# Kernel tuning notes

Measured on AMD Instinct MI355X. Metric: run time of the kernel, lower is better.

Reference implementation:

```python
import jax, jax.numpy as jnp
import numpy as np

HIDDEN = 768
INTER = 2048
N_EXPERTS = 8
TOP_K = 2
SWIGLU_LIMIT = 7.0
N_TOK = 8192


def setup_inputs() -> dict:
    key = jax.random.key(0)
    k_x, k_r, k_gu, k_d = jax.random.split(key, 4)
    x = jax.random.normal(k_x, (N_TOK, HIDDEN), dtype=jnp.float32)
    router_w = jax.random.normal(k_r, (N_EXPERTS, HIDDEN), dtype=jnp.float32) * 0.02
    gate_up_proj = jax.random.normal(k_gu, (N_EXPERTS, 2 * INTER, HIDDEN), dtype=jnp.float32) * 0.02
    down_proj = jax.random.normal(k_d, (N_EXPERTS, HIDDEN, INTER), dtype=jnp.float32) * 0.02
    return {"x": x, "router_w": router_w, "gate_up_proj": gate_up_proj, "down_proj": down_proj}


def reference(x, router_w, gate_up_proj, down_proj):
    # router: [n_tok, E]
    router_logits = x @ router_w.T
    topk_vals, topk_idx = jax.lax.top_k(router_logits, TOP_K)  # [n_tok, k]
    topk_weights = jax.nn.softmax(topk_vals.astype(jnp.float32), axis=-1).astype(x.dtype)

    out = jnp.zeros_like(x)
    # Loop over the small fixed expert set; each expert is a dense GEMM over all
    # tokens, masked by its per-token routing weight (0 for unrouted tokens) —
    # identical math to the original gather/GEMM/scatter dispatch.
    for e in range(N_EXPERTS):
        # per-token weight for expert e (sums slots; each expert appears at most once per token)
        w_e = jnp.sum(jnp.where(topk_idx == e, topk_weights, 0.0), axis=-1)  # [n_tok]
        gate_up = x @ gate_up_proj[e].T  # [n_tok, 2*I]
        gate, up = jnp.split(gate_up, 2, axis=-1)
        up = jnp.minimum(up, SWIGLU_LIMIT)
        mlp_out = (jax.nn.silu(gate) * up) @ down_proj[e].T  # [n_tok, H]
        out = out + mlp_out * w_e[:, None]
    return out
```

## Files before the change

kernel.cpp:

```cpp
#include <hip/hip_runtime.h>
#include <hip/hip_bf16.h>

typedef unsigned short u16;
typedef unsigned int u32;
typedef short bf16x8 __attribute__((ext_vector_type(8)));
typedef float f32x4 __attribute__((ext_vector_type(4)));

#define NTOK 8192
#define HID 768
#define INTER 2048
#define NEXP 8

#define MFMA16(a, b, c) __builtin_amdgcn_mfma_f32_16x16x32_bf16(a, b, c, 0, 0, 0)
#define S_BARRIER() __builtin_amdgcn_s_barrier()
#define WAITVM(n) asm volatile("s_waitcnt vmcnt(" #n ")" ::: "memory")

__device__ __forceinline__ u16 f2bf(float f) {
    u32 u = __builtin_bit_cast(u32, f);
    u32 r = (u + 0x7FFFu + ((u >> 16) & 1u)) >> 16;
    return (u16)r;
}

__device__ __forceinline__ void gld16(const void* g, void* l) {
    __builtin_amdgcn_global_load_lds((const __attribute__((address_space(1))) void*)g,
                                     (__attribute__((address_space(3))) void*)l, 16, 0, 0);
}

__global__ __launch_bounds__(256) void zero_kernel(float4* out4, int n4) {
    int i = blockIdx.x * blockDim.x + threadIdx.x;
    float4 z = {0.f, 0.f, 0.f, 0.f};
    int stride = gridDim.x * blockDim.x;
    for (int k = i; k < n4; k += stride) out4[k] = z;
}

__global__ __launch_bounds__(256) void cvt_kernel(const float* __restrict__ src, u16* __restrict__ dst, int n8) {
    int i = blockIdx.x * blockDim.x + threadIdx.x;
    int stride = gridDim.x * blockDim.x;
    for (; i < n8; i += stride) {
        const float4* s = (const float4*)(src + (size_t)i * 8);
        float4 a = s[0], b = s[1];
        u16 r[8] = {f2bf(a.x), f2bf(a.y), f2bf(a.z), f2bf(a.w),
                    f2bf(b.x), f2bf(b.y), f2bf(b.z), f2bf(b.w)};
        *(uint4*)(dst + (size_t)i * 8) = *(const uint4*)r;
    }
}

__global__ __launch_bounds__(256) void router2(const float* __restrict__ x, const float* __restrict__ rw,
                                               u32* __restrict__ route, float* __restrict__ wslot) {
    int wv = threadIdx.x >> 6, ln = threadIdx.x & 63;
    int t = blockIdx.x * 4 + wv;
    if (t >= NTOK) return;
    float xr[12];
#pragma unroll
    for (int j = 0; j < 12; j++) xr[j] = x[(size_t)t * HID + ln + j * 64];
    float lg[NEXP];
#pragma unroll
    for (int e = 0; e < NEXP; e++) {
        float a = 0.f;
#pragma unroll
        for (int j = 0; j < 12; j++) a += xr[j] * rw[e * HID + ln + j * 64];
#pragma unroll
        for (int off = 32; off; off >>= 1) a += __shfl_xor(a, off);
        lg[e] = a;
    }
    int i0 = 0;
    float v0 = lg[0];
#pragma unroll
    for (int e = 1; e < NEXP; e++)
        if (lg[e] > v0) { v0 = lg[e]; i0 = e; }
    int i1 = -1;
    float v1 = -1e30f;
#pragma unroll
    for (int e = 0; e < NEXP; e++) {
        if (e == i0) continue;
        if (lg[e] > v1) { v1 = lg[e]; i1 = e; }
    }
    float w0 = 1.f / (1.f + __expf(v1 - v0));
    float w1 = 1.f - w0;
    if (ln == 0) {
        wslot[0 * NTOK + t] = w0;
        wslot[1 * NTOK + t] = w1;
        route[t] = (u32)i0 | ((u32)i1 << 8);
    }
}

__global__ __launch_bounds__(1024) void scatter_kernel(const u32* __restrict__ route, int* __restrict__ counts,
                                                       int* __restrict__ tokslot, int* __restrict__ ntiles,
                                                       int* __restrict__ tiledesc) {
    __shared__ int sc[NEXP][1024];
    int tid = threadIdx.x;
    u32 rt[8];
    int cnt[NEXP] = {0, 0, 0, 0, 0, 0, 0, 0};
#pragma unroll
    for (int k = 0; k < 8; k++) {
        rt[k] = route[tid * 8 + k];
        cnt[rt[k] & 255]++;
        cnt[(rt[k] >> 8) & 255]++;
    }
#pragma unroll
    for (int e = 0; e < NEXP; e++) sc[e][tid] = cnt[e];
    __syncthreads();
    for (int off = 1; off < 1024; off <<= 1) {
        int v[NEXP];
#pragma unroll
        for (int e = 0; e < NEXP; e++) v[e] = (tid >= off) ? sc[e][tid - off] : 0;
        __syncthreads();
#pragma unroll
        for (int e = 0; e < NEXP; e++)
            if (tid >= off) sc[e][tid] += v[e];
        __syncthreads();
    }
    int base[NEXP];
#pragma unroll
    for (int e = 0; e < NEXP; e++) base[e] = sc[e][tid] - cnt[e];
#pragma unroll
    for (int k = 0; k < 8; k++) {
        int t = tid * 8 + k;
        int e0 = rt[k] & 255, e1 = (rt[k] >> 8) & 255;
        tokslot[e0 * NTOK + base[e0]] = t;
        base[e0]++;
        tokslot[e1 * NTOK + base[e1]] = t | (1 << 16);
        base[e1]++;
    }
    if (tid == 0) {
        int tot = 0;
        for (int e = 0; e < NEXP; e++) {
            int c = sc[e][1023];
            counts[e] = c;
            int nt = (c + 255) >> 8;
            for (int q = 0; q < nt; q++) tiledesc[tot++] = (e << 8) | q;
        }
        ntiles[0] = tot;
    }
}


#define STG(d, kt)                                           \
    do {                                                     \
        char* base_ = lds + (d)*24576 + (tid << 4);          \
        size_t ko_ = (size_t)(kt)*64;                        \
        gld16(aP[0] + ko_, base_);                           \
        gld16(aP[1] + ko_, base_ + 4096);                    \
        gld16(aP[2] + ko_, base_ + 8192);                    \
        gld16(aP[3] + ko_, base_ + 12288);                   \
        gld16(bP[0] + ko_, base_ + 16384);                   \
        gld16(bP[1] + ko_, base_ + 20480);                   \
    } while (0)

#define PIPE_MB(NKT)                                                      \
    f32x4 acc[8][4];                                                      \
    _Pragma("unroll") for (int m_ = 0; m_ < 8; m_++)                      \
        _Pragma("unroll") for (int n_ = 0; n_ < 4; n_++) acc[m_][n_] = (f32x4)0.f; \
    const int sOff = ((g4 ^ (rsel & 3) ^ ((rsel >> 2) & 3)) << 4);        \
    const int aBase = (wr * 128 + rsel) * 64 + sOff;                      \
    const int bBase = 16384 + (wc * 64 + rsel) * 64 + sOff;               \
    STG(0, 0);                                                            \
    WAITVM(0);                                                            \
    S_BARRIER();                                                          \
    for (int t = 0; t < (NKT); ++t) {                                     \
        if (t + 1 < (NKT)) STG((t + 1) & 1, t + 1);                       \
        const char* Tb = lds + (t & 1) * 24576;                           \
        bf16x8 af[8], bfr[4];                                             \
        _Pragma("unroll") for (int m_ = 0; m_ < 8; m_++)                  \
            af[m_] = *(const bf16x8*)(Tb + aBase + m_ * 1024);            \
        _Pragma("unroll") for (int n_ = 0; n_ < 4; n_++)                  \
            bfr[n_] = *(const bf16x8*)(Tb + bBase + n_ * 1024);           \
        _Pragma("unroll") for (int m_ = 0; m_ < 8; m_++)                  \
            _Pragma("unroll") for (int n_ = 0; n_ < 4; n_++)              \
                acc[m_][n_] = MFMA16(af[m_], bfr[n_], acc[m_][n_]);       \
        WAITVM(0);                                                        \
        S_BARRIER();                                                      \
    }

__global__ __launch_bounds__(256, 2) void gateup_mb(const u16* __restrict__ xb, const u16* __restrict__ gub,
                                                    const int* __restrict__ counts,
                                                    const int* __restrict__ ntiles, const int* __restrict__ tiledesc,
                                                    const int* __restrict__ tokslot, u16* __restrict__ h) {
    if ((int)blockIdx.y >= ntiles[0]) return;
    int td = tiledesc[blockIdx.y];
    int e = td >> 8;
    int cnt = counts[e];
    int row0 = (td & 255) * 256;
    int c0 = blockIdx.x * 64;

    extern __shared__ char lds[];
    int tid = threadIdx.x;
    int wv = tid >> 6, ln = tid & 63;
    int wr = wv >> 1, wc = wv & 1;
    int rsel = ln & 15, g4 = ln >> 4;

    int srow = tid >> 2, sl = tid & 3;
    int sswz = ((sl ^ (srow & 3) ^ ((srow >> 2) & 3)) << 4);
    const char* aP[4];
    const char* bP[2];
#pragma unroll
    for (int c = 0; c < 4; c++) {
        int gr = row0 + c * 64 + srow;
        gr = gr < cnt ? gr : cnt - 1;
        int tok = tokslot[e * NTOK + gr] & 0xFFFF;
        aP[c] = (const char*)xb + (size_t)tok * (HID * 2) + sswz;
    }
#pragma unroll
    for (int c = 0; c < 2; c++) {
        int r = c * 64 + srow;
        int wi = r & 63;
        int b = (wi >> 5) * 2048 + c0 + (r >> 6) * 32 + (wi & 31);
        bP[c] = (const char*)gub + ((size_t)e * 4096 + b) * (HID * 2) + sswz;
    }

    PIPE_MB(HID / 32)

#pragma unroll
    for (int mg = 0; mg < 8; mg++) {
#pragma unroll
        for (int j = 0; j < 4; j++) {
            int gr = row0 + wr * 128 + mg * 16 + g4 * 4 + j;
            if (gr >= cnt) continue;
            int ts = tokslot[e * NTOK + gr];
            int tok = ts & 0xFFFF, slot = ts >> 16;
            u16* hrow = h + (size_t)(slot * NTOK + tok) * INTER;
#pragma unroll
            for (int n = 0; n < 2; n++) {
                float gv = acc[mg][n][j];
                float uv = fminf(acc[mg][n + 2][j], 7.0f);
                float sg = gv / (1.0f + __expf(-gv));
                hrow[c0 + wc * 32 + n * 16 + rsel] = f2bf(sg * uv);
            }
        }
    }
}

__global__ __launch_bounds__(256, 2) void down_mb(const u16* __restrict__ hb, const u16* __restrict__ dnb,
                                                  const int* __restrict__ counts,
                                                  const int* __restrict__ ntiles, const int* __restrict__ tiledesc,
                                                  const int* __restrict__ tokslot,
                                                  const float* __restrict__ wslot, float* __restrict__ out) {
    if ((int)blockIdx.y >= ntiles[0]) return;
    int td = tiledesc[blockIdx.y];
    int e = td >> 8;
    int cnt = counts[e];
    int row0 = (td & 255) * 256;
    int col0 = blockIdx.x * 128;

    extern __shared__ char lds[];
    int tid = threadIdx.x;
    int wv = tid >> 6, ln = tid & 63;
    int wr = wv >> 1, wc = wv & 1;
    int rsel = ln & 15, g4 = ln >> 4;

    int srow = tid >> 2, sl = tid & 3;
    int sswz = ((sl ^ (srow & 3) ^ ((srow >> 2) & 3)) << 4);
    const char* aP[4];
    const char* bP[2];
#pragma unroll
    for (int c = 0; c < 4; c++) {
        int gr = row0 + c * 64 + srow;
        gr = gr < cnt ? gr : cnt - 1;
        int ts = tokslot[e * NTOK + gr];
        aP[c] = (const char*)hb + (size_t)((ts >> 16) * NTOK + (ts & 0xFFFF)) * (INTER * 2) + sswz;
    }
#pragma unroll
    for (int c = 0; c < 2; c++) {
        int r = c * 64 + srow;
        bP[c] = (const char*)dnb + ((size_t)e * HID + col0 + r) * (INTER * 2) + sswz;
    }

    PIPE_MB(INTER / 32)

#pragma unroll
    for (int mg = 0; mg < 8; mg++) {
#pragma unroll
        for (int j = 0; j < 4; j++) {
            int gr = row0 + wr * 128 + mg * 16 + g4 * 4 + j;
            if (gr >= cnt) continue;
            int ts = tokslot[e * NTOK + gr];
            int tok = ts & 0xFFFF, slot = ts >> 16;
            float w = wslot[slot * NTOK + tok];
#pragma unroll
            for (int n = 0; n < 4; n++) {
                int col = col0 + wc * 64 + n * 16 + rsel;
                atomicAdd(&out[(size_t)tok * HID + col], w * acc[mg][n][j]);
            }
        }
    }
}

extern "C" void kernel_launch(void* const* d_in, const int* in_sizes, int n_in,
                              void* d_out, int out_size, void* d_ws, size_t ws_size,
                              hipStream_t stream) {
    const float* x = (const float*)d_in[0];
    const float* rw = (const float*)d_in[1];
    const float* gu = (const float*)d_in[2];
    const float* dn = (const float*)d_in[3];
    float* out = (float*)d_out;
    char* ws = (char*)d_ws;

    int* counts = (int*)(ws + 0);
    int* ntiles = (int*)(ws + 64);
    int* tiledesc = (int*)(ws + 128);
    int* tokslot = (int*)(ws + 512);
    float* wslot = (float*)(ws + 262656);
    u16* xb = (u16*)(ws + 328192);
    u16* gub = (u16*)(ws + 12911104);
    u16* dnb = (u16*)(ws + 63242752);
    u16* hb = (u16*)(ws + 88408576);
    u32* route = (u32*)(ws + 88408576);

    zero_kernel<<<1024, 256, 0, stream>>>((float4*)out, NTOK * HID / 4);
    cvt_kernel<<<2048, 256, 0, stream>>>(x, xb, NTOK * HID / 8);
    cvt_kernel<<<2048, 256, 0, stream>>>(gu, gub, NEXP * 2 * INTER * HID / 8);
    cvt_kernel<<<2048, 256, 0, stream>>>(dn, dnb, NEXP * HID * INTER / 8);
    router2<<<NTOK / 4, 256, 0, stream>>>(x, rw, route, wslot);
    scatter_kernel<<<1, 1024, 0, stream>>>(route, counts, tokslot, ntiles, tiledesc);
    gateup_mb<<<dim3(32, 72), 256, 49152, stream>>>(xb, gub, counts, ntiles, tiledesc, tokslot, hb);
    down_mb<<<dim3(6, 72), 256, 49152, stream>>>(hb, dnb, counts, ntiles, tiledesc, tokslot, wslot, out);
}
```

Before: 343.8 us.

## Fuse output zeroing into router, store h compactly per expert, raise occupancy

The separate output-zeroing kernel is removed, and each router wave now zeroes its token's output row. The intermediate h is stored in expert-sorted compact order, indexed by a per-expert base offset computed in the scatter kernel. Gate-up stores and down-proj A loads therefore become contiguous rows instead of tokslot-indirected scattered rows, and gate-up no longer reads tokslot in its epilogue. Launch bounds are raised to 3 blocks per CU, which may force register spilling given the 32 accumulator vectors per thread.

```diff
diff --git a/kernel.cpp b/kernel.cpp
--- a/kernel.cpp
+++ b/kernel.cpp
@@ -24,13 +24,6 @@
 __device__ __forceinline__ void gld16(const void* g, void* l) {
     __builtin_amdgcn_global_load_lds((const __attribute__((address_space(1))) void*)g,
                                      (__attribute__((address_space(3))) void*)l, 16, 0, 0);
-}
-
-__global__ __launch_bounds__(256) void zero_kernel(float4* out4, int n4) {
-    int i = blockIdx.x * blockDim.x + threadIdx.x;
-    float4 z = {0.f, 0.f, 0.f, 0.f};
-    int stride = gridDim.x * blockDim.x;
-    for (int k = i; k < n4; k += stride) out4[k] = z;
 }
 
 __global__ __launch_bounds__(256) void cvt_kernel(const float* __restrict__ src, u16* __restrict__ dst, int n8) {
@@ -45,11 +38,15 @@
     }
 }
 
-__global__ __launch_bounds__(256) void router2(const float* __restrict__ x, const float* __restrict__ rw,
-                                               u32* __restrict__ route, float* __restrict__ wslot) {
+__global__ __launch_bounds__(256) void router2z(const float* __restrict__ x, const float* __restrict__ rw,
+                                                u32* __restrict__ route, float* __restrict__ wslot,
+                                                float4* __restrict__ out4) {
     int wv = threadIdx.x >> 6, ln = threadIdx.x & 63;
     int t = blockIdx.x * 4 + wv;
     if (t >= NTOK) return;
+    float4 z = {0.f, 0.f, 0.f, 0.f};
+#pragma unroll
+    for (int k = 0; k < 3; k++) out4[(size_t)t * 192 + ln + k * 64] = z;
     float xr[12];
 #pragma unroll
     for (int j = 0; j < 12; j++) xr[j] = x[(size_t)t * HID + ln + j * 64];
@@ -86,7 +83,7 @@
 
 __global__ __launch_bounds__(1024) void scatter_kernel(const u32* __restrict__ route, int* __restrict__ counts,
                                                        int* __restrict__ tokslot, int* __restrict__ ntiles,
-                                                       int* __restrict__ tiledesc) {
+                                                       int* __restrict__ tiledesc, int* __restrict__ ebase) {
     __shared__ int sc[NEXP][1024];
     int tid = threadIdx.x;
     u32 rt[8];
@@ -123,10 +120,12 @@
         base[e1]++;
     }
     if (tid == 0) {
-        int tot = 0;
+        int tot = 0, b = 0;
         for (int e = 0; e < NEXP; e++) {
             int c = sc[e][1023];
             counts[e] = c;
+            ebase[e] = b;
+            b += c;
             int nt = (c + 255) >> 8;
             for (int q = 0; q < nt; q++) tiledesc[tot++] = (e << 8) | q;
         }
@@ -172,14 +171,16 @@
         S_BARRIER();                                                      \
     }
 
-__global__ __launch_bounds__(256, 2) void gateup_mb(const u16* __restrict__ xb, const u16* __restrict__ gub,
+__global__ __launch_bounds__(256, 3) void gateup_mb(const u16* __restrict__ xb, const u16* __restrict__ gub,
                                                     const int* __restrict__ counts,
                                                     const int* __restrict__ ntiles, const int* __restrict__ tiledesc,
-                                                    const int* __restrict__ tokslot, u16* __restrict__ h) {
+                                                    const int* __restrict__ tokslot, const int* __restrict__ ebase,
+                                                    u16* __restrict__ h) {
     if ((int)blockIdx.y >= ntiles[0]) return;
     int td = tiledesc[blockIdx.y];
     int e = td >> 8;
     int cnt = counts[e];
+    int eb = ebase[e];
     int row0 = (td & 255) * 256;
     int c0 = blockIdx.x * 64;
 
@@ -216,9 +217,7 @@
         for (int j = 0; j < 4; j++) {
             int gr = row0 + wr * 128 + mg * 16 + g4 * 4 + j;
             if (gr >= cnt) continue;
-            int ts = tokslot[e * NTOK + gr];
-            int tok = ts & 0xFFFF, slot = ts >> 16;
-            u16* hrow = h + (size_t)(slot * NTOK + tok) * INTER;
+            u16* hrow = h + (size_t)(eb + gr) * INTER;
 #pragma unroll
             for (int n = 0; n < 2; n++) {
                 float gv = acc[mg][n][j];
@@ -230,15 +229,16 @@
     }
 }
 
-__global__ __launch_bounds__(256, 2) void down_mb(const u16* __restrict__ hb, const u16* __restrict__ dnb,
+__global__ __launch_bounds__(256, 3) void down_mb(const u16* __restrict__ hb, const u16* __restrict__ dnb,
                                                   const int* __restrict__ counts,
                                                   const int* __restrict__ ntiles, const int* __restrict__ tiledesc,
-                                                  const int* __restrict__ tokslot,
+                                                  const int* __restrict__ tokslot, const int* __restrict__ ebase,
                                                   const float* __restrict__ wslot, float* __restrict__ out) {
     if ((int)blockIdx.y >= ntiles[0]) return;
     int td = tiledesc[blockIdx.y];
     int e = td >> 8;
     int cnt = counts[e];
+    int eb = ebase[e];
     int row0 = (td & 255) * 256;
     int col0 = blockIdx.x * 128;
 
@@ -256,8 +256,7 @@
     for (int c = 0; c < 4; c++) {
         int gr = row0 + c * 64 + srow;
         gr = gr < cnt ? gr : cnt - 1;
-        int ts = tokslot[e * NTOK + gr];
-        aP[c] = (const char*)hb + (size_t)((ts >> 16) * NTOK + (ts & 0xFFFF)) * (INTER * 2) + sswz;
+        aP[c] = (const char*)hb + (size_t)(eb + gr) * (INTER * 2) + sswz;
     }
 #pragma unroll
     for (int c = 0; c < 2; c++) {
@@ -298,6 +297,7 @@
     int* counts = (int*)(ws + 0);
     int* ntiles = (int*)(ws + 64);
     int* tiledesc = (int*)(ws + 128);
+    int* ebase = (int*)(ws + 448);
     int* tokslot = (int*)(ws + 512);
     float* wslot = (float*)(ws + 262656);
     u16* xb = (u16*)(ws + 328192);
@@ -306,12 +306,11 @@
     u16* hb = (u16*)(ws + 88408576);
     u32* route = (u32*)(ws + 88408576);
 
-    zero_kernel<<<1024, 256, 0, stream>>>((float4*)out, NTOK * HID / 4);
     cvt_kernel<<<2048, 256, 0, stream>>>(x, xb, NTOK * HID / 8);
     cvt_kernel<<<2048, 256, 0, stream>>>(gu, gub, NEXP * 2 * INTER * HID / 8);
     cvt_kernel<<<2048, 256, 0, stream>>>(dn, dnb, NEXP * HID * INTER / 8);
-    router2<<<NTOK / 4, 256, 0, stream>>>(x, rw, route, wslot);
-    scatter_kernel<<<1, 1024, 0, stream>>>(route, counts, tokslot, ntiles, tiledesc);
-    gateup_mb<<<dim3(32, 72), 256, 49152, stream>>>(xb, gub, counts, ntiles, tiledesc, tokslot, hb);
-    down_mb<<<dim3(6, 72), 256, 49152, stream>>>(hb, dnb, counts, ntiles, tiledesc, tokslot, wslot, out);
-}
+    router2z<<<NTOK / 4, 256, 0, stream>>>(x, rw, route, wslot, (float4*)out);
+    scatter_kernel<<<1, 1024, 0, stream>>>(route, counts, tokslot, ntiles, tiledesc, ebase);
+    gateup_mb<<<dim3(32, 72), 256, 49152, stream>>>(xb, gub, counts, ntiles, tiledesc, tokslot, ebase, hb);
+    down_mb<<<dim3(6, 72), 256, 49152, stream>>>(hb, dnb, counts, ntiles, tiledesc, tokslot, ebase, wslot, out);
+}
```

Result: faster. 314.7 us (-8.5%).
